# Kernel optimization log

Measured on AMD Instinct MI355X. Metric: run time of the kernel, lower is better.

Reference implementation:

```python
import jax, jax.numpy as jnp
import numpy as np

MODES = 32
WIDTH = 64
FACTOR = 2
N_LAYERS = 4


def dct_matrix(N):
    # Ortho DCT-II matrix D: dct(x) along last axis = x @ D.T ; idct(y) = y @ D
    n = jnp.arange(N, dtype=jnp.float32)
    k = n[:, None]
    D = jnp.cos(jnp.pi * (n[None, :] + 0.5) * k / N) * jnp.sqrt(2.0 / N)
    D = D.at[0].mul(1.0 / jnp.sqrt(2.0))
    return D


def setup_inputs() -> dict:
    key = jax.random.key(0)
    ks = jax.random.split(key, 16)
    B, M, N, IN_DIM = 4, 256, 256, 12
    hid = WIDTH * FACTOR
    xav_f = jnp.sqrt(2.0 / (WIDTH + WIDTH))  # xavier_normal for (in,out,modes)
    inp = {
        'x': jax.random.normal(ks[0], (B, M, N, IN_DIM), jnp.float32),
        'W_in': jax.random.normal(ks[1], (WIDTH, IN_DIM), jnp.float32) * (1.0 / jnp.sqrt(IN_DIM)),
        'b_in': jnp.zeros((WIDTH,), jnp.float32),
        'fw0': jax.random.normal(ks[2], (N_LAYERS, WIDTH, WIDTH, MODES), jnp.float32) * xav_f,
        'fw1': jax.random.normal(ks[3], (N_LAYERS, WIDTH, WIDTH, MODES), jnp.float32) * xav_f,
        'ffW1': jax.random.normal(ks[4], (N_LAYERS, hid, WIDTH), jnp.float32) * (1.0 / jnp.sqrt(WIDTH)),
        'ffb1': jnp.zeros((N_LAYERS, hid), jnp.float32),
        'ffW2': jax.random.normal(ks[5], (N_LAYERS, WIDTH, hid), jnp.float32) * (1.0 / jnp.sqrt(hid)),
        'ffb2': jnp.zeros((N_LAYERS, WIDTH), jnp.float32),
        'W_o1': jax.random.normal(ks[6], (128, WIDTH), jnp.float32) * (1.0 / jnp.sqrt(WIDTH)),
        'b_o1': jnp.zeros((128,), jnp.float32),
        'W_o2': jax.random.normal(ks[7], (1, 128), jnp.float32) * (1.0 / jnp.sqrt(128.0)),
        'b_o2': jnp.zeros((1,), jnp.float32),
    }
    return inp


def forward_fourier(x, w0, w1, DM, DN):
    # x: [B, M, N, I] channels-last -> [B, I, M, N]
    x = jnp.transpose(x, (0, 3, 1, 2))
    # --- y direction: DCT along N, truncated mode mix, IDCT ---
    x_fty = jnp.einsum('bimn,kn->bimk', x, DN)            # dct, [B,I,M,N]
    xy_m = jnp.einsum('bixy,ioy->boxy', x_fty[..., :MODES], w0)  # [B,O,M,modes]
    xy = jnp.einsum('boxy,yn->boxn', xy_m, DN[:MODES, :])        # idct of zero-padded spectrum
    # --- x direction: DCT along M ---
    x2 = jnp.swapaxes(x, -1, -2)                          # [B,I,N,M]
    x_ftx = jnp.einsum('binm,km->bink', x2, DM)
    xx_m = jnp.einsum('bixy,ioy->boxy', x_ftx[..., :MODES], w1)  # [B,O,N,modes]
    xx = jnp.einsum('boxy,ym->boxm', xx_m, DM[:MODES, :])        # [B,O,N,M]
    xx = jnp.swapaxes(xx, -1, -2)                         # [B,O,M,N]
    out = xx + xy
    return jnp.transpose(out, (0, 2, 3, 1))               # [B,M,N,O]


def feed_forward(h, W1, b1, W2, b2):
    h = jax.nn.relu(h @ W1.T + b1)
    return h @ W2.T + b2


def reference(x, W_in, b_in, fw0, fw1, ffW1, ffb1, ffW2, ffb2, W_o1, b_o1, W_o2, b_o2):
    B, M, N, _ = x.shape
    DM = dct_matrix(M)
    DN = dct_matrix(N)
    x = x @ W_in.T + b_in                                  # in_proj, [B,M,N,width]
    b = x
    for i in range(N_LAYERS):
        h = forward_fourier(x, fw0[i], fw1[i], DM, DN)
        b = feed_forward(h, ffW1[i], ffb1[i], ffW2[i], ffb2[i])
        x = x + b
    # use_fork=False: out applied to the LAST backcast b
    o = jax.nn.relu(b @ W_o1.T + b_o1) * 0 + (b @ W_o1.T + b_o1)  # WNLinear has no activation
    o = b @ W_o1.T + b_o1
    forecast = o @ W_o2.T + b_o2                           # [B,M,N,1]
    return forecast
```

## Files before the change

### kernel.cpp

```cpp
#include <hip/hip_runtime.h>
#include <hip/hip_bf16.h>
#include <math.h>

#define BATCH 4
#define MMDIM 256
#define NNDIM 256
#define CH 64
#define NMODES 32
#define HID 128
#define NLAYERS 4
#define XPLANE 16777216L

typedef __attribute__((ext_vector_type(8))) short bfrag;
typedef __attribute__((ext_vector_type(8))) ushort u16x8;
typedef __attribute__((ext_vector_type(4))) float f32x4;

__device__ inline ushort f2bf(float x) {
    union { float f; uint u; } v; v.f = x;
    uint r = v.u + 0x7fff + ((v.u >> 16) & 1);
    return (ushort)(r >> 16);
}
__device__ inline float bf2f(ushort h) {
    union { uint u; float f; } v; v.u = (uint)h << 16; return v.f;
}
__device__ inline void split(float v, ushort& hi, ushort& lo) {
    __hip_bfloat16 h = __float2bfloat16(v);
    hi = __builtin_bit_cast(ushort, h);
    lo = __builtin_bit_cast(ushort, __float2bfloat16(v - __bfloat162float(h)));
}
__device__ inline ushort f2bf_hw(float v) {
    return __builtin_bit_cast(ushort, __float2bfloat16(v));
}
#define MFMA __builtin_amdgcn_mfma_f32_16x16x32_bf16


__global__ __launch_bounds__(256) void k_Tfrag(ushort* __restrict__ Tf) {
    int idx = blockIdx.x * 256 + threadIdx.x;
    int j = idx & 7, lane = (idx >> 3) & 63, ks = (idx >> 9) & 7, yt = idx >> 12;
    int k = yt * 16 + (lane & 15);
    int n = ks * 32 + ((lane >> 4) << 3) + j;
    double v = cos(M_PI * (n + 0.5) * (double)k / 256.0) * 0.08838834764831845;
    if (k == 0) v *= 0.7071067811865476;
    float vf = (float)v;
    ushort hh = f2bf(vf);
    Tf[idx] = hh; Tf[idx + 8192] = f2bf(vf - bf2f(hh));
}

__global__ __launch_bounds__(256) void k_Ttfrag(ushort* __restrict__ Ttf) {
    int idx = blockIdx.x * 256 + threadIdx.x;
    int j = idx & 7, lane = (idx >> 3) & 63, at = idx >> 9;
    int k = ((lane >> 4) << 3) + j;
    int n = at * 16 + (lane & 15);
    double v = cos(M_PI * (n + 0.5) * (double)k / 256.0) * 0.08838834764831845;
    if (k == 0) v *= 0.7071067811865476;
    float vf = (float)v;
    ushort hh = f2bf(vf);
    Ttf[idx] = hh; Ttf[idx + 8192] = f2bf(vf - bf2f(hh));
}

__global__ __launch_bounds__(256) void k_wt(const float* __restrict__ fw0, const float* __restrict__ fw1,
                                            float* __restrict__ wt01) {
    int idx = blockIdx.x * 256 + threadIdx.x;
    const float* fw = (idx < 524288) ? fw0 : fw1;
    int i2 = idx & 524287;
    int l = i2 >> 17, r = i2 & 131071;
    int y = r >> 12, i = (r >> 6) & 63, o = r & 63;
    wt01[idx] = fw[((l * 64 + i) * 64 + o) * 32 + y];
}

__global__ __launch_bounds__(256) void k_wfrag(const float* __restrict__ W,
                                               ushort* __restrict__ hi, ushort* __restrict__ lo,
                                               int N, int K) {
    int idx = blockIdx.x * 256 + threadIdx.x;
    int per_l = N * K;
    int l = idx / per_l, r = idx % per_l;
    int jj = r & 7, lane = (r >> 3) & 63;
    int ks = (r >> 9) % (K >> 5);
    int nt = r / (512 * (K >> 5));
    int row = nt * 16 + (lane & 15);
    int col = ks * 32 + ((lane >> 4) << 3) + jj;
    float v = W[(long)l * per_l + row * K + col];
    ushort h = f2bf(v);
    hi[idx] = h;
    lo[idx] = f2bf(v - bf2f(h));
}

__global__ void k_head(const float* __restrict__ W_o1, const float* __restrict__ b_o1,
                       const float* __restrict__ W_o2, const float* __restrict__ b_o2,
                       float* __restrict__ Weff, float* __restrict__ beff) {
    int c = threadIdx.x;
    float acc = 0.f;
    for (int j = 0; j < 128; j++) acc += W_o2[j] * W_o1[j * 64 + c];
    Weff[c] = acc;
    if (c == 0) {
        float bb = 0.f;
        for (int j = 0; j < 128; j++) bb += W_o2[j] * b_o1[j];
        beff[0] = bb + b_o2[0];
    }
}

__global__ __launch_bounds__(256) void k_inproj_bf(const float* __restrict__ xin,
                                                   const float* __restrict__ W_in,
                                                   const float* __restrict__ b_in,
                                                   ushort* __restrict__ xbf) {
    __shared__ __align__(16) ushort tile[2][64][72];
    int t = threadIdx.x;
    int bid = blockIdx.x;
    int b = bid >> 10, m = (bid >> 2) & 255, n0 = (bid & 3) * 64;
    int c = t & 63, ng = t >> 6;
    long pbase = (long)(b * 256 + m) * 256 + n0;
    float w[12];
#pragma unroll
    for (int d = 0; d < 12; d++) w[d] = W_in[c * 12 + d];
    float bc = b_in[c];
#pragma unroll 4
    for (int i = 0; i < 16; i++) {
        int nl = ng * 16 + i;
        const float* xr = xin + (pbase + nl) * 12;
        float acc = bc;
#pragma unroll
        for (int d = 0; d < 12; d++) acc += xr[d] * w[d];
        ushort hh, ll;
        split(acc, hh, ll);
        tile[0][c][nl] = hh;
        tile[1][c][nl] = ll;
    }
    __syncthreads();
    int c2 = t >> 2, ch = t & 3;
#pragma unroll
    for (int pl = 0; pl < 2; pl++) {
        const ushort* s = &tile[pl][c2][ch * 16];
        u16x8 v0 = *(const u16x8*)s;
        u16x8 v1 = *(const u16x8*)(s + 8);
        ushort* dst = xbf + (long)pl * XPLANE + ((long)(b * 256 + m) * 64 + c2) * 256 + n0 + ch * 16;
        *(u16x8*)dst = v0; *(u16x8*)(dst + 8) = v1;
    }
}

__global__ __launch_bounds__(256) void k_tx(const ushort* __restrict__ src, ushort* __restrict__ dst) {
    __shared__ __align__(16) ushort tl[64][72];
    int t = threadIdx.x;
    int bid = blockIdx.x;
    int ntile = bid & 3, mt = (bid >> 2) & 3, c = (bid >> 4) & 63, b = (bid >> 10) & 3, pl = bid >> 12;
    int m0 = mt * 64, n0 = ntile * 64;
    const ushort* sp = src + (long)pl * XPLANE;
    ushort* dp = dst + (long)pl * XPLANE;
    {
        int row = t >> 2, ch = (t & 3) * 16;
        const ushort* p = sp + ((long)(b * 256 + m0 + row) * 64 + c) * 256 + n0 + ch;
        u16x8 v0 = *(const u16x8*)p;
        u16x8 v1 = *(const u16x8*)(p + 8);
#pragma unroll
        for (int k = 0; k < 8; k++) tl[ch + k][row] = v0[k];
#pragma unroll
        for (int k = 0; k < 8; k++) tl[ch + 8 + k][row] = v1[k];
    }
    __syncthreads();
    {
        int nrow = t >> 2, mch = (t & 3) * 16;
        const ushort* s = &tl[nrow][mch];
        u16x8 v0 = *(const u16x8*)s;
        u16x8 v1 = *(const u16x8*)(s + 8);
        ushort* p = dp + ((long)(b * 256 + n0 + nrow) * 64 + c) * 256 + m0 + mch;
        *(u16x8*)p = v0; *(u16x8*)(p + 8) = v1;
    }
}

__global__ __launch_bounds__(512) void k_spec(const ushort* __restrict__ xbf_y,
                                              const ushort* __restrict__ xbf_x,
                                              const ushort* __restrict__ Tf,
                                              const ushort* __restrict__ Ttf,
                                              const float* __restrict__ wt_y,
                                              const float* __restrict__ wt_x,
                                              float* __restrict__ hy,
                                              ushort* __restrict__ hx) {
    __shared__ float Xs[2][32][68];
    __shared__ __align__(16) ushort Xmb[2][2][64][40];
    int t = threadIdx.x;
    int lane = t & 63, wv = t >> 6, l15 = lane & 15, l4 = lane >> 4;
    int bid = blockIdx.x;
    int xpath = bid >> 9;
    int lb = bid & 511;
    int fp = lb & 127, b = lb >> 7;
    int s_ = wv >> 2;
    const ushort* xbf = xpath ? xbf_x : xbf_y;
    const float* wt = xpath ? wt_x : wt_y;

    {
        const ushort* xb = xbf + ((long)(b * 256 + fp * 2 + s_)) * 16384;
        f32x4 a0 = {0.f, 0.f, 0.f, 0.f}, a1 = {0.f, 0.f, 0.f, 0.f};
        int c0 = (wv & 3) * 16;
#pragma unroll
        for (int ks = 0; ks < 8; ks++) {
            const ushort* bp = xb + (c0 + l15) * 256 + ks * 32 + l4 * 8;
            bfrag bhi = *(const bfrag*)bp;
            bfrag blo = *(const bfrag*)(bp + XPLANE);
            const ushort* ap0 = Tf + (long)((0 * 8 + ks) * 64 + lane) * 8;
            const ushort* ap1 = Tf + (long)((1 * 8 + ks) * 64 + lane) * 8;
            bfrag a0h = *(const bfrag*)ap0, a0l = *(const bfrag*)(ap0 + 8192);
            bfrag a1h = *(const bfrag*)ap1, a1l = *(const bfrag*)(ap1 + 8192);
            a0 = MFMA(a0h, bhi, a0, 0, 0, 0);
            a0 = MFMA(a0h, blo, a0, 0, 0, 0);
            a0 = MFMA(a0l, bhi, a0, 0, 0, 0);
            a1 = MFMA(a1h, bhi, a1, 0, 0, 0);
            a1 = MFMA(a1h, blo, a1, 0, 0, 0);
            a1 = MFMA(a1l, bhi, a1, 0, 0, 0);
        }
#pragma unroll
        for (int r = 0; r < 4; r++) {
            Xs[s_][l4 * 4 + r][c0 + l15] = a0[r];
            Xs[s_][16 + l4 * 4 + r][c0 + l15] = a1[r];
        }
    }
    __syncthreads();

    {
        int og = t & 15, y = t >> 4;
        const float* wb = wt + (long)y * 4096 + og * 4;
        f32x4 A0 = {0.f, 0.f, 0.f, 0.f}, A1 = {0.f, 0.f, 0.f, 0.f};
#pragma unroll 8
        for (int i = 0; i < 64; i++) {
            float4 wv4 = *(const float4*)(wb + i * 64);
            float x0 = Xs[0][y][i];
            float x1 = Xs[1][y][i];
            A0.x += x0 * wv4.x; A0.y += x0 * wv4.y; A0.z += x0 * wv4.z; A0.w += x0 * wv4.w;
            A1.x += x1 * wv4.x; A1.y += x1 * wv4.y; A1.z += x1 * wv4.z; A1.w += x1 * wv4.w;
        }
#pragma unroll
        for (int e = 0; e < 4; e++) {
            ushort hh, ll;
            split(A0[e], hh, ll);
            Xmb[0][0][og * 4 + e][y] = hh;
            Xmb[0][1][og * 4 + e][y] = ll;
            split(A1[e], hh, ll);
            Xmb[1][0][og * 4 + e][y] = hh;
            Xmb[1][1][og * 4 + e][y] = ll;
        }
    }
    __syncthreads();

    bfrag vbh[4], vbl[4];
#pragma unroll
    for (int ot = 0; ot < 4; ot++) {
        vbh[ot] = *(const bfrag*)(&Xmb[s_][0][ot * 16 + l15][l4 * 8]);
        vbl[ot] = *(const bfrag*)(&Xmb[s_][1][ot * 16 + l15][l4 * 8]);
    }
    int f = fp * 2 + s_;
#pragma unroll
    for (int ai = 0; ai < 4; ai++) {
        int at = (wv & 3) * 4 + ai;
        const ushort* ap = Ttf + (long)(at * 64 + lane) * 8;
        bfrag th = *(const bfrag*)ap, tl_ = *(const bfrag*)(ap + 8192);
#pragma unroll
        for (int ot = 0; ot < 4; ot++) {
            f32x4 acc = {0.f, 0.f, 0.f, 0.f};
            acc = MFMA(th, vbh[ot], acc, 0, 0, 0);
            acc = MFMA(th, vbl[ot], acc, 0, 0, 0);
            acc = MFMA(tl_, vbh[ot], acc, 0, 0, 0);
            int arow = at * 16 + l4 * 4;
            if (!xpath) {
                float* op = hy + (long)b * 4194304 + (long)f * 16384 + (long)arow * 64 + ot * 16 + l15;
#pragma unroll
                for (int r = 0; r < 4; r++) op[r * 64] = acc[r];
            } else {
                ushort* op = hx + (long)b * 4194304 + (long)f * 16384 + (long)arow * 64 + ot * 16 + l15;
#pragma unroll
                for (int r = 0; r < 4; r++) op[r * 64] = f2bf_hw(acc[r]);
            }
        }
    }
}

#define ASW 136
__global__ __launch_bounds__(256) void k_ff(const float* __restrict__ hy,
                                            const ushort* __restrict__ hx,
                                            ushort* __restrict__ xbfw,
                                            const ushort* __restrict__ W1hi, const ushort* __restrict__ W1lo,
                                            const float* __restrict__ b1,
                                            const ushort* __restrict__ W2hi, const ushort* __restrict__ W2lo,
                                            const float* __restrict__ b2,
                                            const float* __restrict__ Weff, const float* __restrict__ beff,
                                            float* __restrict__ out, int last) {
    __shared__ __align__(16) ushort Asb[2][64][ASW];
    int t = threadIdx.x;
    int lane = t & 63, wv = t >> 6;
    int l15 = lane & 15, l4 = lane >> 4;
    long p0 = (long)blockIdx.x * 64;
    int b = (int)(p0 >> 16), m = (int)((p0 >> 8) & 255), n0 = (int)(p0 & 255);

    f32x4 acc1[8];
#pragma unroll
    for (int nt = 0; nt < 8; nt++) acc1[nt] = (f32x4){0.f, 0.f, 0.f, 0.f};
#pragma unroll
    for (int ks = 0; ks < 2; ks++) {
        int px = wv * 16 + l15;
        const float* hp = hy + (p0 + px) * 64 + ks * 32 + l4 * 8;
        float4 h0 = *(const float4*)hp;
        float4 h1 = *(const float4*)(hp + 4);
        long xoff = ((long)b * 65536 + (long)(n0 + px) * 256 + m) * 64 + ks * 32 + l4 * 8;
        u16x8 hx8 = *(const u16x8*)(hx + xoff);
        bfrag ahi, alo;
#pragma unroll
        for (int j = 0; j < 8; j++) {
            float v = ((j < 4) ? (&h0.x)[j] : (&h1.x)[j - 4]) + bf2f(hx8[j]);
            ushort hh, ll;
            split(v, hh, ll);
            ahi[j] = (short)hh; alo[j] = (short)ll;
        }
#pragma unroll
        for (int nt = 0; nt < 8; nt++) {
            long off = (long)((nt * 2 + ks) * 64 + lane) * 8;
            bfrag bhi = *(const bfrag*)(W1hi + off);
            bfrag blo = *(const bfrag*)(W1lo + off);
            acc1[nt] = MFMA(ahi, bhi, acc1[nt], 0, 0, 0);
            acc1[nt] = MFMA(ahi, blo, acc1[nt], 0, 0, 0);
            acc1[nt] = MFMA(alo, bhi, acc1[nt], 0, 0, 0);
        }
    }
#pragma unroll
    for (int nt = 0; nt < 8; nt++) {
        float bj = b1[nt * 16 + l15];
        int j = nt * 16 + l15;
#pragma unroll
        for (int r = 0; r < 4; r++) {
            float v = fmaxf(acc1[nt][r] + bj, 0.f);
            int px = wv * 16 + l4 * 4 + r;
            ushort hh, ll;
            split(v, hh, ll);
            Asb[0][px][j] = hh;
            Asb[1][px][j] = ll;
        }
    }
    __syncthreads();

    f32x4 acc2[4];
#pragma unroll
    for (int nt = 0; nt < 4; nt++) acc2[nt] = (f32x4){0.f, 0.f, 0.f, 0.f};
#pragma unroll
    for (int ks = 0; ks < 4; ks++) {
        bfrag ahi = *(const bfrag*)(&Asb[0][wv * 16 + l15][ks * 32 + l4 * 8]);
        bfrag alo = *(const bfrag*)(&Asb[1][wv * 16 + l15][ks * 32 + l4 * 8]);
#pragma unroll
        for (int nt = 0; nt < 4; nt++) {
            long off = (long)((nt * 4 + ks) * 64 + lane) * 8;
            bfrag bhi = *(const bfrag*)(W2hi + off);
            bfrag blo = *(const bfrag*)(W2lo + off);
            acc2[nt] = MFMA(ahi, bhi, acc2[nt], 0, 0, 0);
            acc2[nt] = MFMA(ahi, blo, acc2[nt], 0, 0, 0);
            acc2[nt] = MFMA(alo, bhi, acc2[nt], 0, 0, 0);
        }
    }

    if (last) {
        float be = beff[0];
#pragma unroll
        for (int r = 0; r < 4; r++) {
            float v = 0.f;
#pragma unroll
            for (int nt = 0; nt < 4; nt++) {
                int c = nt * 16 + l15;
                v += (acc2[nt][r] + b2[c]) * Weff[c];
            }
            v += __shfl_xor(v, 1, 64);
            v += __shfl_xor(v, 2, 64);
            v += __shfl_xor(v, 4, 64);
            v += __shfl_xor(v, 8, 64);
            if (l15 == 0) out[p0 + wv * 16 + l4 * 4 + r] = v + be;
        }
    } else {
        __syncthreads();
        ushort* tile = &Asb[0][0][0];
        int c2 = t >> 2, ch = t & 3;
#pragma unroll
        for (int pl = 0; pl < 2; pl++) {
            const ushort* src = xbfw + (long)pl * XPLANE + ((long)(b * 256 + m) * 64 + c2) * 256 + n0 + ch * 16;
            u16x8 v0 = *(const u16x8*)src;
            u16x8 v1 = *(const u16x8*)(src + 8);
            ushort* d = tile + (pl * 64 + c2) * 72 + ch * 16;
            *(u16x8*)d = v0; *(u16x8*)(d + 8) = v1;
        }
        __syncthreads();
#pragma unroll
        for (int nt = 0; nt < 4; nt++) {
            int c = nt * 16 + l15;
            float bc = b2[c];
#pragma unroll
            for (int r = 0; r < 4; r++) {
                int nl = wv * 16 + l4 * 4 + r;
                float res = bf2f(tile[(0 * 64 + c) * 72 + nl]) + bf2f(tile[(1 * 64 + c) * 72 + nl]);
                float v = res + acc2[nt][r] + bc;
                ushort hh, ll;
                split(v, hh, ll);
                tile[(0 * 64 + c) * 72 + nl] = hh;
                tile[(1 * 64 + c) * 72 + nl] = ll;
            }
        }
        __syncthreads();
#pragma unroll
        for (int pl = 0; pl < 2; pl++) {
            const ushort* s = tile + (pl * 64 + c2) * 72 + ch * 16;
            u16x8 v0 = *(const u16x8*)s;
            u16x8 v1 = *(const u16x8*)(s + 8);
            ushort* dst = xbfw + (long)pl * XPLANE + ((long)(b * 256 + m) * 64 + c2) * 256 + n0 + ch * 16;
            *(u16x8*)dst = v0; *(u16x8*)(dst + 8) = v1;
        }
    }
}


extern "C" void kernel_launch(void* const* d_in, const int* in_sizes, int n_in,
                              void* d_out, int out_size, void* d_ws, size_t ws_size,
                              hipStream_t stream) {
    const float* x_in = (const float*)d_in[0];
    const float* W_in = (const float*)d_in[1];
    const float* b_in = (const float*)d_in[2];
    const float* fw0  = (const float*)d_in[3];
    const float* fw1  = (const float*)d_in[4];
    const float* ffW1 = (const float*)d_in[5];
    const float* ffb1 = (const float*)d_in[6];
    const float* ffW2 = (const float*)d_in[7];
    const float* ffb2 = (const float*)d_in[8];
    const float* W_o1 = (const float*)d_in[9];
    const float* b_o1 = (const float*)d_in[10];
    const float* W_o2 = (const float*)d_in[11];
    const float* b_o2 = (const float*)d_in[12];
    float* out = (float*)d_out;

    float* ws   = (float*)d_ws;
    float* w0t  = ws;
    float* w1t  = w0t + 524288;
    float* Weff = w1t + 524288;
    float* beff = Weff + 64;
    float* h_y  = beff + 64;
    ushort* h_x = (ushort*)(h_y + 16777216);
    ushort* Tfrag  = h_x + 16777216;
    ushort* Ttfrag = Tfrag + 16384;
    ushort* W1f_hi = Ttfrag + 16384;
    ushort* W1f_lo = W1f_hi + 32768;
    ushort* W2f_hi = W1f_lo + 32768;
    ushort* W2f_lo = W2f_hi + 32768;
    ushort* xbf_y  = W2f_lo + 32768;
    ushort* xbf_x  = xbf_y + 2 * XPLANE;

    k_Tfrag<<<32, 256, 0, stream>>>(Tfrag);
    k_Ttfrag<<<32, 256, 0, stream>>>(Ttfrag);
    k_wt<<<4096, 256, 0, stream>>>(fw0, fw1, w0t);
    k_wfrag<<<(NLAYERS * HID * CH) / 256, 256, 0, stream>>>(ffW1, W1f_hi, W1f_lo, HID, CH);
    k_wfrag<<<(NLAYERS * CH * HID) / 256, 256, 0, stream>>>(ffW2, W2f_hi, W2f_lo, CH, HID);
    k_head<<<1, 64, 0, stream>>>(W_o1, b_o1, W_o2, b_o2, Weff, beff);
    k_inproj_bf<<<4096, 256, 0, stream>>>(x_in, W_in, b_in, xbf_y);

    for (int l = 0; l < NLAYERS; l++) {
        k_tx<<<8192, 256, 0, stream>>>(xbf_y, xbf_x);
        k_spec<<<1024, 512, 0, stream>>>(xbf_y, xbf_x, Tfrag, Ttfrag,
                                         w0t + (long)l * 131072, w1t + (long)l * 131072,
                                         h_y, h_x);
        k_ff<<<4096, 256, 0, stream>>>(h_y, h_x, xbf_y,
            W1f_hi + (long)l * HID * CH, W1f_lo + (long)l * HID * CH,
            ffb1 + (long)l * HID,
            W2f_hi + (long)l * CH * HID, W2f_lo + (long)l * CH * HID,
            ffb2 + (long)l * CH,
            Weff, beff, out, (l == NLAYERS - 1) ? 1 : 0);
    }
}
```

Baseline: 616.5 us.

## Fuse y-direction inverse DCT into feed-forward kernel, storing truncated spectrum

The spectral kernel no longer expands the y-path mode-mixed spectrum back to a full fp32 field. It writes only the 32-mode hi/lo bf16 split coefficients. The feed-forward kernel now does the inverse DCT for its 64-pixel tile with MFMAs into shared memory before its usual work. This removes a large fp32 intermediate write and read per layer, at the cost of extra MFMA work and shared memory in k_ff, which may lower occupancy.

```diff
diff --git a/kernel.cpp b/kernel.cpp
--- a/kernel.cpp
+++ b/kernel.cpp
@@ -172,7 +172,7 @@
                                               const ushort* __restrict__ Ttf,
                                               const float* __restrict__ wt_y,
                                               const float* __restrict__ wt_x,
-                                              float* __restrict__ hy,
+                                              ushort* __restrict__ xmy,
                                               ushort* __restrict__ hx) {
     __shared__ float Xs[2][32][68];
     __shared__ __align__(16) ushort Xmb[2][2][64][40];
@@ -239,6 +239,16 @@
     }
     __syncthreads();
 
+    if (!xpath) {
+        int r = t & 255, s2 = t >> 8;
+        int pl = r >> 7, c = (r >> 1) & 63, yh = (r & 1) * 16;
+        long f2 = fp * 2 + s2;
+        ushort* dst = xmy + ((long)(b * 256 + f2) * 2 + pl) * 2048 + c * 32 + yh;
+        *(u16x8*)dst = *(const u16x8*)&Xmb[s2][pl][c][yh];
+        *(u16x8*)(dst + 8) = *(const u16x8*)&Xmb[s2][pl][c][yh + 8];
+        return;
+    }
+
     bfrag vbh[4], vbl[4];
 #pragma unroll
     for (int ot = 0; ot < 4; ot++) {
@@ -258,22 +268,17 @@
             acc = MFMA(th, vbl[ot], acc, 0, 0, 0);
             acc = MFMA(tl_, vbh[ot], acc, 0, 0, 0);
             int arow = at * 16 + l4 * 4;
-            if (!xpath) {
-                float* op = hy + (long)b * 4194304 + (long)f * 16384 + (long)arow * 64 + ot * 16 + l15;
-#pragma unroll
-                for (int r = 0; r < 4; r++) op[r * 64] = acc[r];
-            } else {
-                ushort* op = hx + (long)b * 4194304 + (long)f * 16384 + (long)arow * 64 + ot * 16 + l15;
-#pragma unroll
-                for (int r = 0; r < 4; r++) op[r * 64] = f2bf_hw(acc[r]);
-            }
+            ushort* op = hx + (long)b * 4194304 + (long)f * 16384 + (long)arow * 64 + ot * 16 + l15;
+#pragma unroll
+            for (int r = 0; r < 4; r++) op[r * 64] = f2bf_hw(acc[r]);
         }
     }
 }
 
 #define ASW 136
-__global__ __launch_bounds__(256) void k_ff(const float* __restrict__ hy,
+__global__ __launch_bounds__(256) void k_ff(const ushort* __restrict__ xmy,
                                             const ushort* __restrict__ hx,
+                                            const ushort* __restrict__ Ttf,
                                             ushort* __restrict__ xbfw,
                                             const ushort* __restrict__ W1hi, const ushort* __restrict__ W1lo,
                                             const float* __restrict__ b1,
@@ -281,6 +286,7 @@
                                             const float* __restrict__ b2,
                                             const float* __restrict__ Weff, const float* __restrict__ beff,
                                             float* __restrict__ out, int last) {
+    __shared__ __align__(16) float hyt[64][68];
     __shared__ __align__(16) ushort Asb[2][64][ASW];
     int t = threadIdx.x;
     int lane = t & 63, wv = t >> 6;
@@ -288,13 +294,34 @@
     long p0 = (long)blockIdx.x * 64;
     int b = (int)(p0 >> 16), m = (int)((p0 >> 8) & 255), n0 = (int)(p0 & 255);
 
+    {
+        const ushort* xm = xmy + ((long)(b * 256 + m) * 2) * 2048;
+        int at = (n0 >> 4) + wv;
+        const ushort* ap = Ttf + (long)(at * 64 + lane) * 8;
+        bfrag th = *(const bfrag*)ap, tl_ = *(const bfrag*)(ap + 8192);
+#pragma unroll
+        for (int ot = 0; ot < 4; ot++) {
+            const ushort* xp = xm + (ot * 16 + l15) * 32 + l4 * 8;
+            bfrag xh = *(const bfrag*)xp;
+            bfrag xl = *(const bfrag*)(xp + 2048);
+            f32x4 acc = {0.f, 0.f, 0.f, 0.f};
+            acc = MFMA(th, xh, acc, 0, 0, 0);
+            acc = MFMA(th, xl, acc, 0, 0, 0);
+            acc = MFMA(tl_, xh, acc, 0, 0, 0);
+#pragma unroll
+            for (int r = 0; r < 4; r++)
+                hyt[wv * 16 + l4 * 4 + r][ot * 16 + l15] = acc[r];
+        }
+    }
+    __syncthreads();
+
     f32x4 acc1[8];
 #pragma unroll
     for (int nt = 0; nt < 8; nt++) acc1[nt] = (f32x4){0.f, 0.f, 0.f, 0.f};
 #pragma unroll
     for (int ks = 0; ks < 2; ks++) {
         int px = wv * 16 + l15;
-        const float* hp = hy + (p0 + px) * 64 + ks * 32 + l4 * 8;
+        const float* hp = &hyt[px][ks * 32 + l4 * 8];
         float4 h0 = *(const float4*)hp;
         float4 h1 = *(const float4*)(hp + 4);
         long xoff = ((long)b * 65536 + (long)(n0 + px) * 256 + m) * 64 + ks * 32 + l4 * 8;
@@ -431,8 +458,8 @@
     float* w1t  = w0t + 524288;
     float* Weff = w1t + 524288;
     float* beff = Weff + 64;
-    float* h_y  = beff + 64;
-    ushort* h_x = (ushort*)(h_y + 16777216);
+    ushort* xmy = (ushort*)(beff + 64);
+    ushort* h_x = xmy + 4194304;
     ushort* Tfrag  = h_x + 16777216;
     ushort* Ttfrag = Tfrag + 16384;
     ushort* W1f_hi = Ttfrag + 16384;
@@ -454,8 +481,8 @@
         k_tx<<<8192, 256, 0, stream>>>(xbf_y, xbf_x);
         k_spec<<<1024, 512, 0, stream>>>(xbf_y, xbf_x, Tfrag, Ttfrag,
                                          w0t + (long)l * 131072, w1t + (long)l * 131072,
-                                         h_y, h_x);
-        k_ff<<<4096, 256, 0, stream>>>(h_y, h_x, xbf_y,
+                                         xmy, h_x);
+        k_ff<<<4096, 256, 0, stream>>>(xmy, h_x, Ttfrag, xbf_y,
             W1f_hi + (long)l * HID * CH, W1f_lo + (long)l * HID * CH,
             ffb1 + (long)l * HID,
             W2f_hi + (long)l * CH * HID, W2f_lo + (long)l * CH * HID,
```

Measured after the change: 607.7 us. No clear change (-1.4%).
